# Kernel tuning notes

Hardware: AMD Instinct MI355X
Metric: run time of the kernel (lower is better)

The kernel has to match this reference:

```python
import jax, jax.numpy as jnp
import numpy as np

B = 131072

def _lin(x, w, b):
    return x @ w.T + b

def setup_inputs() -> dict:
    key = jax.random.key(0)
    ks = jax.random.split(key, 32)
    def rn(k, shape, scale=0.05):
        return jax.random.normal(k, shape, dtype=jnp.float32) * scale
    inp = {
        "x": rn(ks[0], (B, 256), 1.0),
        "w": rn(ks[1], (B, 36), 1.0),
        "h0": rn(ks[2], (B, 32), 1.0),
        "c0": rn(ks[3], (B, 32), 1.0),
        "fc1_w": rn(ks[4], (128, 256)), "fc1_b": rn(ks[5], (128,)),
        "fc1a_w": rn(ks[6], (128, 164)), "fc1a_b": rn(ks[7], (128,)),
        "fc1b_w": rn(ks[8], (128, 128)), "fc1b_b": rn(ks[9], (128,)),
        "w_game": rn(ks[10], (1, 12), 1.0),
        "fc1c_w": rn(ks[11], (64, 140)), "fc1c_b": rn(ks[12], (64,)),
        "fc2_w": rn(ks[13], (32, 64)), "fc2_b": rn(ks[14], (32,)),
        "fc3_w": rn(ks[15], (32, 32)), "fc3_b": rn(ks[16], (32,)),
        "w_ih": rn(ks[17], (128, 32)), "w_hh": rn(ks[18], (128, 32)),
        "b_ih": rn(ks[19], (128,)), "b_hh": rn(ks[20], (128,)),
        "fc4_w": rn(ks[21], (32, 32)), "fc4_b": rn(ks[22], (32,)),
        "fc5_w": rn(ks[23], (1, 32)), "fc5_b": rn(ks[24], (1,)),
    }
    return inp

def reference(x, w, h0, c0, fc1_w, fc1_b, fc1a_w, fc1a_b, fc1b_w, fc1b_b,
              w_game, fc1c_w, fc1c_b, fc2_w, fc2_b, fc3_w, fc3_b,
              w_ih, w_hh, b_ih, b_hh, fc4_w, fc4_b, fc5_w, fc5_b):
    b = x.shape[0]
    h = jax.nn.relu(_lin(x, fc1_w, fc1_b))                      # [B,128]
    h = jnp.concatenate([h, w], axis=-1)                        # [B,164]
    h = jax.nn.relu(_lin(h, fc1a_w, fc1a_b))                    # [B,128]
    h = jax.nn.relu(_lin(h, fc1b_w, fc1b_b))                    # [B,128]
    wg = jnp.broadcast_to(w_game.reshape(1, 12), (b, 12))
    h = jnp.concatenate([h, wg], axis=-1)                       # [B,140]
    h = jax.nn.relu(_lin(h, fc1c_w, fc1c_b))                    # [B,64]
    h = jax.nn.relu(_lin(h, fc2_w, fc2_b))                      # [B,32]
    h = jax.nn.relu(_lin(h, fc3_w, fc3_b))                      # [B,32]
    # LSTMCell step (torch gate order: input, forget, cell, output)
    gates = _lin(h, w_ih, b_ih) + _lin(h0, w_hh, b_hh)          # [B,128]
    i_g, f_g, g_g, o_g = jnp.split(gates, 4, axis=-1)
    c_new = jax.nn.sigmoid(f_g) * c0 + jax.nn.sigmoid(i_g) * jnp.tanh(g_g)
    h_new = jax.nn.sigmoid(o_g) * jnp.tanh(c_new)               # [B,32]
    out = jax.nn.relu(_lin(h_new, fc4_w, fc4_b))                # [B,32]
    out = _lin(out, fc5_w, fc5_b)                               # [B,1]
    return jax.nn.sigmoid(out)
```

## Files before the change

### kernel.cpp

```cpp
#include <hip/hip_runtime.h>
#include <hip/hip_bf16.h>


typedef __bf16 bf16x8 __attribute__((ext_vector_type(8)));
typedef float  f32x4  __attribute__((ext_vector_type(4)));
typedef int    i32x4  __attribute__((ext_vector_type(4)));

#define MFMA16(A, B, C) __builtin_amdgcn_mfma_f32_16x16x32_bf16((A), (B), (C), 0, 0, 0)

#define WOFF_FC1    0
#define WOFF_FC1A_H 32768
#define WOFF_FC1B   49152
#define WOFF_FC1C   65536
#define LDS_ELEMS   73728
#define WOFF_FC1A_W 73728
#define WOFF_FC2    81920
#define WOFF_FC3    83968
#define WOFF_WIH    84992
#define WOFF_WHH    89088
#define WOFF_FC4    93184
#define WTOT        94208
#define BOFF_FC1  0
#define BOFF_FC1A 128
#define BOFF_FC1B 256
#define BOFF_FC1C 384
#define BOFF_FC2  448
#define BOFF_FC3  480
#define BOFF_LSTM 512
#define BOFF_FC4  640
#define BTOT      672

__device__ __forceinline__ void conv_frag(int rel, const float* __restrict__ src,
                                          __bf16* __restrict__ dst,
                                          int ns, int Krow, int kbase, int klim, int perm) {
    int j    = rel & 7;
    int lane = (rel >> 3) & 63;
    int fs   = rel >> 9;
    int s    = fs % ns;
    int t    = fs / ns;
    int gq   = lane >> 4;
    int n    = 16 * t + (lane & 15);
    int k    = perm ? (16 * (2 * s + (j >> 2)) + 4 * gq + (j & 3))
                    : (32 * s + 8 * gq + j);
    float v  = (k < klim) ? src[n * Krow + kbase + k] : 0.f;
    dst[rel] = (__bf16)v;
}

__global__ void prep_kernel(const float* __restrict__ fc1w,  const float* __restrict__ fc1b,
                            const float* __restrict__ fc1aw, const float* __restrict__ fc1ab,
                            const float* __restrict__ fc1bw, const float* __restrict__ fc1bb,
                            const float* __restrict__ wgame, const float* __restrict__ fc1cw,
                            const float* __restrict__ fc1cb, const float* __restrict__ fc2w,
                            const float* __restrict__ fc2b,  const float* __restrict__ fc3w,
                            const float* __restrict__ fc3b,  const float* __restrict__ wih,
                            const float* __restrict__ whh,   const float* __restrict__ bih,
                            const float* __restrict__ bhh,   const float* __restrict__ fc4w,
                            const float* __restrict__ fc4b,
                            __bf16* __restrict__ wsw, float* __restrict__ wsb) {
    int idx = blockIdx.x * 256 + threadIdx.x;
    if (idx < WTOT) {
        if      (idx < WOFF_FC1A_H) conv_frag(idx - WOFF_FC1,    fc1w,  wsw + WOFF_FC1,    8, 256,   0, 256, 0);
        else if (idx < WOFF_FC1B)   conv_frag(idx - WOFF_FC1A_H, fc1aw, wsw + WOFF_FC1A_H, 4, 164,   0, 128, 1);
        else if (idx < WOFF_FC1C)   conv_frag(idx - WOFF_FC1B,   fc1bw, wsw + WOFF_FC1B,   4, 128,   0, 128, 1);
        else if (idx < WOFF_FC1A_W) conv_frag(idx - WOFF_FC1C,   fc1cw, wsw + WOFF_FC1C,   4, 140,   0, 128, 1);
        else if (idx < WOFF_FC2)    conv_frag(idx - WOFF_FC1A_W, fc1aw, wsw + WOFF_FC1A_W, 2, 164, 128,  36, 0);
        else if (idx < WOFF_FC3)    conv_frag(idx - WOFF_FC2,    fc2w,  wsw + WOFF_FC2,    2,  64,   0,  64, 1);
        else if (idx < WOFF_WIH)    conv_frag(idx - WOFF_FC3,    fc3w,  wsw + WOFF_FC3,    1,  32,   0,  32, 1);
        else if (idx < WOFF_WHH)    conv_frag(idx - WOFF_WIH,    wih,   wsw + WOFF_WIH,    1,  32,   0,  32, 1);
        else if (idx < WOFF_FC4)    conv_frag(idx - WOFF_WHH,    whh,   wsw + WOFF_WHH,    1,  32,   0,  32, 0);
        else                        conv_frag(idx - WOFF_FC4,    fc4w,  wsw + WOFF_FC4,    1,  32,   0,  32, 1);
    } else if (idx < WTOT + BTOT) {
        int bi = idx - WTOT;
        float v;
        if      (bi < 128) v = fc1b[bi];
        else if (bi < 256) v = fc1ab[bi - 128];
        else if (bi < 384) v = fc1bb[bi - 256];
        else if (bi < 448) {
            int n = bi - 384;
            v = fc1cb[n];
            for (int q = 0; q < 12; ++q) v += fc1cw[n * 140 + 128 + q] * wgame[q];
        }
        else if (bi < 480) v = fc2b[bi - 448];
        else if (bi < 512) v = fc3b[bi - 480];
        else if (bi < 640) { int n = bi - 512; v = bih[n] + bhh[n]; }
        else               v = fc4b[bi - 640];
        wsb[bi] = v;
    }
}

__device__ __forceinline__ bf16x8 ld8f(const float* __restrict__ p) {
    f32x4 a = *(const f32x4*)p;
    f32x4 b = *(const f32x4*)(p + 4);
    bf16x8 r;
    r[0] = (__bf16)a[0]; r[1] = (__bf16)a[1]; r[2] = (__bf16)a[2]; r[3] = (__bf16)a[3];
    r[4] = (__bf16)b[0]; r[5] = (__bf16)b[1]; r[6] = (__bf16)b[2]; r[7] = (__bf16)b[3];
    return r;
}

__device__ __forceinline__ bf16x8 ld4f_masked(const float* __restrict__ p, bool on) {
    f32x4 v = {0.f, 0.f, 0.f, 0.f};
    if (on) v = *(const f32x4*)p;
    bf16x8 r;
    r[0] = (__bf16)v[0]; r[1] = (__bf16)v[1]; r[2] = (__bf16)v[2]; r[3] = (__bf16)v[3];
    r[4] = (__bf16)0.f;  r[5] = (__bf16)0.f;  r[6] = (__bf16)0.f;  r[7] = (__bf16)0.f;
    return r;
}

__device__ __forceinline__ bf16x8 packrelu(const f32x4* a, int s) {
    bf16x8 r;
#pragma unroll
    for (int j = 0; j < 8; ++j) {
        float v = a[2 * s + (j >> 2)][j & 3];
        r[j] = (__bf16)fmaxf(v, 0.f);
    }
    return r;
}

__device__ __forceinline__ float sigm(float v)  { return 1.f / (1.f + __expf(-v)); }
__device__ __forceinline__ float tanh_(float v) { return 1.f - 2.f / (1.f + __expf(2.f * v)); }

__global__ __launch_bounds__(1024, 4) void fused_mlp_lstm(
        const float* __restrict__ x,  const float* __restrict__ w,
        const float* __restrict__ h0, const float* __restrict__ c0,
        const float* __restrict__ fc5w, const float* __restrict__ fc5b,
        const __bf16* __restrict__ wsw, const float* __restrict__ wsb,
        float* __restrict__ out) {
    __shared__ __align__(16) __bf16 slds[LDS_ELEMS];

    const int tid     = threadIdx.x;
    const int lane    = tid & 63;
    const int gq      = lane >> 4;
    const int mr      = lane & 15;
    const int rowbase = blockIdx.x * 256 + (tid >> 6) * 16;
    const int row     = rowbase + mr;

    {
        const i32x4* gs = (const i32x4*)wsw;
        i32x4*       sd = (i32x4*)slds;
#pragma unroll
        for (int i = 0; i < 9; ++i) sd[i * 1024 + tid] = gs[i * 1024 + tid];
    }
    __syncthreads();

    const bf16x8* Wfc1  = (const bf16x8*)(slds + WOFF_FC1);
    const bf16x8* Wf1aH = (const bf16x8*)(slds + WOFF_FC1A_H);
    const bf16x8* Wfc1b = (const bf16x8*)(slds + WOFF_FC1B);
    const bf16x8* Wfc1c = (const bf16x8*)(slds + WOFF_FC1C);
    const bf16x8* Wf1aW = (const bf16x8*)(wsw + WOFF_FC1A_W);
    const bf16x8* Wfc2  = (const bf16x8*)(wsw + WOFF_FC2);
    const bf16x8* Wfc3  = (const bf16x8*)(wsw + WOFF_FC3);
    const bf16x8* Wwih  = (const bf16x8*)(wsw + WOFF_WIH);
    const bf16x8* Wwhh  = (const bf16x8*)(wsw + WOFF_WHH);
    const bf16x8* Wfc4  = (const bf16x8*)(wsw + WOFF_FC4);

    bf16x8 h1f[4];
    {
        f32x4 acc1[8];
#pragma unroll
        for (int t = 0; t < 8; ++t)
            acc1[t] = *(const f32x4*)(wsb + BOFF_FC1 + 16 * t + 4 * gq);
        const float* xrow = x + row * 256 + 8 * gq;
#pragma unroll
        for (int p = 0; p < 4; ++p) {
            bf16x8 a0 = ld8f(xrow + 64 * p);
            bf16x8 a1 = ld8f(xrow + 64 * p + 32);
#pragma unroll
            for (int t = 0; t < 8; ++t)
                acc1[t] = MFMA16(Wfc1[(t * 8 + 2 * p) * 64 + lane], a0, acc1[t]);
#pragma unroll
            for (int t = 0; t < 8; ++t)
                acc1[t] = MFMA16(Wfc1[(t * 8 + 2 * p + 1) * 64 + lane], a1, acc1[t]);
        }
#pragma unroll
        for (int s = 0; s < 4; ++s) h1f[s] = packrelu(acc1, s);
    }

    bf16x8 h2f[4];
    {
        bf16x8 wxa0 = ld8f(w + row * 36 + 8 * gq);
        bf16x8 wxa1 = ld4f_masked(w + row * 36 + 32, gq == 0);
        f32x4 acc2[8];
#pragma unroll
        for (int t = 0; t < 8; ++t)
            acc2[t] = *(const f32x4*)(wsb + BOFF_FC1A + 16 * t + 4 * gq);
#pragma unroll
        for (int s = 0; s < 4; ++s)
#pragma unroll
            for (int t = 0; t < 8; ++t)
                acc2[t] = MFMA16(Wf1aH[(t * 4 + s) * 64 + lane], h1f[s], acc2[t]);
#pragma unroll
        for (int t = 0; t < 8; ++t) {
            acc2[t] = MFMA16(Wf1aW[(t * 2 + 0) * 64 + lane], wxa0, acc2[t]);
            acc2[t] = MFMA16(Wf1aW[(t * 2 + 1) * 64 + lane], wxa1, acc2[t]);
        }
#pragma unroll
        for (int s = 0; s < 4; ++s) h2f[s] = packrelu(acc2, s);
    }

    bf16x8 h3f[4];
    {
        f32x4 acc3[8];
#pragma unroll
        for (int t = 0; t < 8; ++t)
            acc3[t] = *(const f32x4*)(wsb + BOFF_FC1B + 16 * t + 4 * gq);
#pragma unroll
        for (int s = 0; s < 4; ++s)
#pragma unroll
            for (int t = 0; t < 8; ++t)
                acc3[t] = MFMA16(Wfc1b[(t * 4 + s) * 64 + lane], h2f[s], acc3[t]);
#pragma unroll
        for (int s = 0; s < 4; ++s) h3f[s] = packrelu(acc3, s);
    }

    bf16x8 h0f  = ld8f(h0 + row * 32 + 8 * gq);
    f32x4  c0r0 = *(const f32x4*)(c0 + row * 32 + 4 * gq);
    f32x4  c0r1 = *(const f32x4*)(c0 + row * 32 + 16 + 4 * gq);

    bf16x8 h4f[2];
    {
        f32x4 acc4[4];
#pragma unroll
        for (int t = 0; t < 4; ++t)
            acc4[t] = *(const f32x4*)(wsb + BOFF_FC1C + 16 * t + 4 * gq);
#pragma unroll
        for (int s = 0; s < 4; ++s)
#pragma unroll
            for (int t = 0; t < 4; ++t)
                acc4[t] = MFMA16(Wfc1c[(t * 4 + s) * 64 + lane], h3f[s], acc4[t]);
#pragma unroll
        for (int s = 0; s < 2; ++s) h4f[s] = packrelu(acc4, s);
    }

    bf16x8 h5f;
    {
        f32x4 acc5[2];
#pragma unroll
        for (int t = 0; t < 2; ++t)
            acc5[t] = *(const f32x4*)(wsb + BOFF_FC2 + 16 * t + 4 * gq);
#pragma unroll
        for (int s = 0; s < 2; ++s)
#pragma unroll
            for (int t = 0; t < 2; ++t)
                acc5[t] = MFMA16(Wfc2[(t * 2 + s) * 64 + lane], h4f[s], acc5[t]);
        h5f = packrelu(acc5, 0);
    }

    bf16x8 h6f;
    {
        f32x4 acc6[2];
#pragma unroll
        for (int t = 0; t < 2; ++t)
            acc6[t] = *(const f32x4*)(wsb + BOFF_FC3 + 16 * t + 4 * gq);
#pragma unroll
        for (int t = 0; t < 2; ++t)
            acc6[t] = MFMA16(Wfc3[t * 64 + lane], h5f, acc6[t]);
        h6f = packrelu(acc6, 0);
    }

    bf16x8 hnf;
    {
        f32x4 accg[8];
#pragma unroll
        for (int t = 0; t < 8; ++t)
            accg[t] = *(const f32x4*)(wsb + BOFF_LSTM + 16 * t + 4 * gq);
#pragma unroll
        for (int t = 0; t < 8; ++t)
            accg[t] = MFMA16(Wwih[t * 64 + lane], h6f, accg[t]);
#pragma unroll
        for (int t = 0; t < 8; ++t)
            accg[t] = MFMA16(Wwhh[t * 64 + lane], h0f, accg[t]);
#pragma unroll
        for (int t2 = 0; t2 < 2; ++t2) {
            f32x4 cc = t2 ? c0r1 : c0r0;
#pragma unroll
            for (int r = 0; r < 4; ++r) {
                float ig = accg[t2][r];
                float fg = accg[2 + t2][r];
                float gg = accg[4 + t2][r];
                float og = accg[6 + t2][r];
                float cn = sigm(fg) * cc[r] + sigm(ig) * tanh_(gg);
                hnf[t2 * 4 + r] = (__bf16)(sigm(og) * tanh_(cn));
            }
        }
    }

    f32x4 acco[2];
#pragma unroll
    for (int t = 0; t < 2; ++t)
        acco[t] = *(const f32x4*)(wsb + BOFF_FC4 + 16 * t + 4 * gq);
#pragma unroll
    for (int t = 0; t < 2; ++t)
        acco[t] = MFMA16(Wfc4[t * 64 + lane], hnf, acco[t]);

    f32x4 w5a = *(const f32x4*)(fc5w + 4 * gq);
    f32x4 w5b = *(const f32x4*)(fc5w + 16 + 4 * gq);
    float p = 0.f;
#pragma unroll
    for (int r = 0; r < 4; ++r) {
        p += fmaxf(acco[0][r], 0.f) * w5a[r];
        p += fmaxf(acco[1][r], 0.f) * w5b[r];
    }
    p += __shfl_xor(p, 16);
    p += __shfl_xor(p, 32);
    float res = sigm(p + fc5b[0]);
    if (lane < 16) out[rowbase + lane] = res;
}

extern "C" void kernel_launch(void* const* d_in, const int* in_sizes, int n_in,
                              void* d_out, int out_size, void* d_ws, size_t ws_size,
                              hipStream_t stream) {
    const float* x     = (const float*)d_in[0];
    const float* w     = (const float*)d_in[1];
    const float* h0    = (const float*)d_in[2];
    const float* c0    = (const float*)d_in[3];
    const float* fc1w  = (const float*)d_in[4];
    const float* fc1b  = (const float*)d_in[5];
    const float* fc1aw = (const float*)d_in[6];
    const float* fc1ab = (const float*)d_in[7];
    const float* fc1bw = (const float*)d_in[8];
    const float* fc1bb = (const float*)d_in[9];
    const float* wgame = (const float*)d_in[10];
    const float* fc1cw = (const float*)d_in[11];
    const float* fc1cb = (const float*)d_in[12];
    const float* fc2w  = (const float*)d_in[13];
    const float* fc2b  = (const float*)d_in[14];
    const float* fc3w  = (const float*)d_in[15];
    const float* fc3b  = (const float*)d_in[16];
    const float* wih   = (const float*)d_in[17];
    const float* whh   = (const float*)d_in[18];
    const float* bih   = (const float*)d_in[19];
    const float* bhh   = (const float*)d_in[20];
    const float* fc4w  = (const float*)d_in[21];
    const float* fc4b  = (const float*)d_in[22];
    const float* fc5w  = (const float*)d_in[23];
    const float* fc5b  = (const float*)d_in[24];

    __bf16* wsw = (__bf16*)d_ws;
    float*  wsb = (float*)((char*)d_ws + WTOT * sizeof(__bf16));
    (void)ws_size; (void)n_in; (void)out_size;

    const int Btot = in_sizes[0] / 256;

    prep_kernel<<<(WTOT + BTOT + 255) / 256, 256, 0, stream>>>(
        fc1w, fc1b, fc1aw, fc1ab, fc1bw, fc1bb, wgame, fc1cw, fc1cb,
        fc2w, fc2b, fc3w, fc3b, wih, whh, bih, bhh, fc4w, fc4b, wsw, wsb);

    fused_mlp_lstm<<<Btot / 256, 1024, 0, stream>>>(
        x, w, h0, c0, fc5w, fc5b, wsw, wsb, (float*)d_out);
}
```

Baseline: 61.42 us.

## Split fused MLP-LSTM into three kernels with LDS-resident weights

Splits the single fused kernel into three stage kernels (fc1, fc1a+fc1b, tail through LSTM and output). Each stage keeps only its own weights in LDS, and each wave processes two 16-row tiles so every weight fragment read from LDS feeds two MFMAs. The aim is to cut LDS footprint per block, which raises occupancy, and to keep the tail weights out of global memory. The cost is a bf16 round-trip of the h1 and h3 activations through workspace (tens of MB of extra traffic) plus extra launches. The old fused kernel is kept as a fallback when the workspace is too small.

```diff
diff --git a/kernel.cpp b/kernel.cpp
--- a/kernel.cpp
+++ b/kernel.cpp
@@ -12,7 +12,6 @@
 #define WOFF_FC1A_H 32768
 #define WOFF_FC1B   49152
 #define WOFF_FC1C   65536
-#define LDS_ELEMS   73728
 #define WOFF_FC1A_W 73728
 #define WOFF_FC2    81920
 #define WOFF_FC3    83968
@@ -29,6 +28,10 @@
 #define BOFF_LSTM 512
 #define BOFF_FC4  640
 #define BTOT      672
+
+#define H1_BYTE_OFF 192512ull
+#define HACT_BYTES  33554432ull
+#define WS_REQUIRED (H1_BYTE_OFF + 2ull * HACT_BYTES)
 
 __device__ __forceinline__ void conv_frag(int rel, const float* __restrict__ src,
                                           __bf16* __restrict__ dst,
@@ -119,6 +122,310 @@
 __device__ __forceinline__ float sigm(float v)  { return 1.f / (1.f + __expf(-v)); }
 __device__ __forceinline__ float tanh_(float v) { return 1.f - 2.f / (1.f + __expf(2.f * v)); }
 
+__global__ __launch_bounds__(512, 2) void k_l1(
+        const float* __restrict__ x, const __bf16* __restrict__ wsw,
+        const float* __restrict__ wsb, __bf16* __restrict__ h1ws) {
+    __shared__ __align__(16) __bf16 slds[32768];
+    const int tid  = threadIdx.x;
+    const int lane = tid & 63;
+    const int wv   = tid >> 6;
+    const int gq   = lane >> 4;
+    const int mr   = lane & 15;
+    {
+        const i32x4* gs = (const i32x4*)(wsw + WOFF_FC1);
+        i32x4*       sd = (i32x4*)slds;
+#pragma unroll
+        for (int i = 0; i < 8; ++i) sd[i * 512 + tid] = gs[i * 512 + tid];
+    }
+    __syncthreads();
+    const bf16x8* Wfc1 = (const bf16x8*)slds;
+
+    const int rowbase = blockIdx.x * 256 + wv * 32;
+    const int rowA = rowbase + mr, rowB = rowA + 16;
+    f32x4 aA[8], aB[8];
+#pragma unroll
+    for (int t = 0; t < 8; ++t) {
+        f32x4 bv = *(const f32x4*)(wsb + BOFF_FC1 + 16 * t + 4 * gq);
+        aA[t] = bv; aB[t] = bv;
+    }
+    const float* xrA = x + rowA * 256 + 8 * gq;
+    const float* xrB = x + rowB * 256 + 8 * gq;
+#pragma unroll
+    for (int p = 0; p < 4; ++p) {
+        bf16x8 a0A = ld8f(xrA + 64 * p);
+        bf16x8 a0B = ld8f(xrB + 64 * p);
+        bf16x8 a1A = ld8f(xrA + 64 * p + 32);
+        bf16x8 a1B = ld8f(xrB + 64 * p + 32);
+#pragma unroll
+        for (int t = 0; t < 8; ++t) {
+            bf16x8 wf = Wfc1[(t * 8 + 2 * p) * 64 + lane];
+            aA[t] = MFMA16(wf, a0A, aA[t]);
+            aB[t] = MFMA16(wf, a0B, aB[t]);
+        }
+#pragma unroll
+        for (int t = 0; t < 8; ++t) {
+            bf16x8 wf = Wfc1[(t * 8 + 2 * p + 1) * 64 + lane];
+            aA[t] = MFMA16(wf, a1A, aA[t]);
+            aB[t] = MFMA16(wf, a1B, aB[t]);
+        }
+    }
+    const int rb = rowbase >> 4;
+#pragma unroll
+    for (int s = 0; s < 4; ++s) {
+        *(bf16x8*)(h1ws + ((rb * 4 + s) * 512)       + lane * 8) = packrelu(aA, s);
+        *(bf16x8*)(h1ws + (((rb + 1) * 4 + s) * 512) + lane * 8) = packrelu(aB, s);
+    }
+}
+
+__global__ __launch_bounds__(512, 2) void k_l1ab(
+        const float* __restrict__ w, const __bf16* __restrict__ wsw,
+        const float* __restrict__ wsb, const __bf16* __restrict__ h1ws,
+        __bf16* __restrict__ h3ws) {
+    __shared__ __align__(16) __bf16 slds[40960];
+    const int tid  = threadIdx.x;
+    const int lane = tid & 63;
+    const int wv   = tid >> 6;
+    const int gq   = lane >> 4;
+    const int mr   = lane & 15;
+    const int rowbase = blockIdx.x * 256 + wv * 32;
+    const int rowA = rowbase + mr, rowB = rowA + 16;
+    const int rb = rowbase >> 4;
+
+    bf16x8 h1fA[4], h1fB[4];
+#pragma unroll
+    for (int s = 0; s < 4; ++s) {
+        h1fA[s] = *(const bf16x8*)(h1ws + ((rb * 4 + s) * 512)       + lane * 8);
+        h1fB[s] = *(const bf16x8*)(h1ws + (((rb + 1) * 4 + s) * 512) + lane * 8);
+    }
+    bf16x8 wxa0 = ld8f(w + rowA * 36 + 8 * gq);
+    bf16x8 wxb0 = ld8f(w + rowB * 36 + 8 * gq);
+    bf16x8 wxa1 = ld4f_masked(w + rowA * 36 + 32, gq == 0);
+    bf16x8 wxb1 = ld4f_masked(w + rowB * 36 + 32, gq == 0);
+
+    {
+        const i32x4* g1 = (const i32x4*)(wsw + WOFF_FC1A_H);
+        const i32x4* g2 = (const i32x4*)(wsw + WOFF_FC1A_W);
+        i32x4*       sd = (i32x4*)slds;
+#pragma unroll
+        for (int i = 0; i < 8; ++i) sd[i * 512 + tid] = g1[i * 512 + tid];
+#pragma unroll
+        for (int i = 0; i < 2; ++i) sd[4096 + i * 512 + tid] = g2[i * 512 + tid];
+    }
+    __syncthreads();
+    const bf16x8* Wf1aH = (const bf16x8*)(slds);
+    const bf16x8* Wfc1b = (const bf16x8*)(slds + 16384);
+    const bf16x8* Wf1aW = (const bf16x8*)(slds + 32768);
+
+    f32x4 aA[8], aB[8];
+#pragma unroll
+    for (int t = 0; t < 8; ++t) {
+        f32x4 bv = *(const f32x4*)(wsb + BOFF_FC1A + 16 * t + 4 * gq);
+        aA[t] = bv; aB[t] = bv;
+    }
+#pragma unroll
+    for (int s = 0; s < 4; ++s)
+#pragma unroll
+        for (int t = 0; t < 8; ++t) {
+            bf16x8 wf = Wf1aH[(t * 4 + s) * 64 + lane];
+            aA[t] = MFMA16(wf, h1fA[s], aA[t]);
+            aB[t] = MFMA16(wf, h1fB[s], aB[t]);
+        }
+#pragma unroll
+    for (int t = 0; t < 8; ++t) {
+        bf16x8 wf0 = Wf1aW[(t * 2 + 0) * 64 + lane];
+        bf16x8 wf1 = Wf1aW[(t * 2 + 1) * 64 + lane];
+        aA[t] = MFMA16(wf0, wxa0, aA[t]);
+        aB[t] = MFMA16(wf0, wxb0, aB[t]);
+        aA[t] = MFMA16(wf1, wxa1, aA[t]);
+        aB[t] = MFMA16(wf1, wxb1, aB[t]);
+    }
+    bf16x8 h2fA[4], h2fB[4];
+#pragma unroll
+    for (int s = 0; s < 4; ++s) { h2fA[s] = packrelu(aA, s); h2fB[s] = packrelu(aB, s); }
+
+    f32x4 bA[8], bB[8];
+#pragma unroll
+    for (int t = 0; t < 8; ++t) {
+        f32x4 bv = *(const f32x4*)(wsb + BOFF_FC1B + 16 * t + 4 * gq);
+        bA[t] = bv; bB[t] = bv;
+    }
+#pragma unroll
+    for (int s = 0; s < 4; ++s)
+#pragma unroll
+        for (int t = 0; t < 8; ++t) {
+            bf16x8 wf = Wfc1b[(t * 4 + s) * 64 + lane];
+            bA[t] = MFMA16(wf, h2fA[s], bA[t]);
+            bB[t] = MFMA16(wf, h2fB[s], bB[t]);
+        }
+#pragma unroll
+    for (int s = 0; s < 4; ++s) {
+        *(bf16x8*)(h3ws + ((rb * 4 + s) * 512)       + lane * 8) = packrelu(bA, s);
+        *(bf16x8*)(h3ws + (((rb + 1) * 4 + s) * 512) + lane * 8) = packrelu(bB, s);
+    }
+}
+
+__global__ __launch_bounds__(512, 2) void k_tail(
+        const float* __restrict__ h0, const float* __restrict__ c0,
+        const float* __restrict__ fc5w, const float* __restrict__ fc5b,
+        const __bf16* __restrict__ wsw, const float* __restrict__ wsb,
+        const __bf16* __restrict__ h3ws, float* __restrict__ out) {
+    __shared__ __align__(16) __bf16 slds[28672];
+    const int tid  = threadIdx.x;
+    const int lane = tid & 63;
+    const int wv   = tid >> 6;
+    const int gq   = lane >> 4;
+    const int mr   = lane & 15;
+    const int rowbase = blockIdx.x * 256 + wv * 32;
+    const int rowA = rowbase + mr, rowB = rowA + 16;
+    const int rb = rowbase >> 4;
+
+    bf16x8 h3fA[4], h3fB[4];
+#pragma unroll
+    for (int s = 0; s < 4; ++s) {
+        h3fA[s] = *(const bf16x8*)(h3ws + ((rb * 4 + s) * 512)       + lane * 8);
+        h3fB[s] = *(const bf16x8*)(h3ws + (((rb + 1) * 4 + s) * 512) + lane * 8);
+    }
+    bf16x8 h0fA = ld8f(h0 + rowA * 32 + 8 * gq);
+    bf16x8 h0fB = ld8f(h0 + rowB * 32 + 8 * gq);
+    f32x4  cA0 = *(const f32x4*)(c0 + rowA * 32 + 4 * gq);
+    f32x4  cA1 = *(const f32x4*)(c0 + rowA * 32 + 16 + 4 * gq);
+    f32x4  cB0 = *(const f32x4*)(c0 + rowB * 32 + 4 * gq);
+    f32x4  cB1 = *(const f32x4*)(c0 + rowB * 32 + 16 + 4 * gq);
+
+    {
+        const i32x4* gs = (const i32x4*)(wsw + WOFF_FC1C);
+        i32x4*       sd = (i32x4*)slds;
+#pragma unroll
+        for (int i = 0; i < 7; ++i) sd[i * 512 + tid] = gs[i * 512 + tid];
+    }
+    __syncthreads();
+    const bf16x8* Wfc1c = (const bf16x8*)(slds);
+    const bf16x8* Wfc2  = (const bf16x8*)(slds + 16384);
+    const bf16x8* Wfc3  = (const bf16x8*)(slds + 18432);
+    const bf16x8* Wwih  = (const bf16x8*)(slds + 19456);
+    const bf16x8* Wwhh  = (const bf16x8*)(slds + 23552);
+    const bf16x8* Wfc4  = (const bf16x8*)(slds + 27648);
+
+    bf16x8 h4fA[2], h4fB[2];
+    {
+        f32x4 aA[4], aB[4];
+#pragma unroll
+        for (int t = 0; t < 4; ++t) {
+            f32x4 bv = *(const f32x4*)(wsb + BOFF_FC1C + 16 * t + 4 * gq);
+            aA[t] = bv; aB[t] = bv;
+        }
+#pragma unroll
+        for (int s = 0; s < 4; ++s)
+#pragma unroll
+            for (int t = 0; t < 4; ++t) {
+                bf16x8 wf = Wfc1c[(t * 4 + s) * 64 + lane];
+                aA[t] = MFMA16(wf, h3fA[s], aA[t]);
+                aB[t] = MFMA16(wf, h3fB[s], aB[t]);
+            }
+#pragma unroll
+        for (int s = 0; s < 2; ++s) { h4fA[s] = packrelu(aA, s); h4fB[s] = packrelu(aB, s); }
+    }
+    bf16x8 h5fA, h5fB;
+    {
+        f32x4 aA[2], aB[2];
+#pragma unroll
+        for (int t = 0; t < 2; ++t) {
+            f32x4 bv = *(const f32x4*)(wsb + BOFF_FC2 + 16 * t + 4 * gq);
+            aA[t] = bv; aB[t] = bv;
+        }
+#pragma unroll
+        for (int s = 0; s < 2; ++s)
+#pragma unroll
+            for (int t = 0; t < 2; ++t) {
+                bf16x8 wf = Wfc2[(t * 2 + s) * 64 + lane];
+                aA[t] = MFMA16(wf, h4fA[s], aA[t]);
+                aB[t] = MFMA16(wf, h4fB[s], aB[t]);
+            }
+        h5fA = packrelu(aA, 0); h5fB = packrelu(aB, 0);
+    }
+    bf16x8 h6fA, h6fB;
+    {
+        f32x4 aA[2], aB[2];
+#pragma unroll
+        for (int t = 0; t < 2; ++t) {
+            f32x4 bv = *(const f32x4*)(wsb + BOFF_FC3 + 16 * t + 4 * gq);
+            aA[t] = bv; aB[t] = bv;
+        }
+#pragma unroll
+        for (int t = 0; t < 2; ++t) {
+            bf16x8 wf = Wfc3[t * 64 + lane];
+            aA[t] = MFMA16(wf, h5fA, aA[t]);
+            aB[t] = MFMA16(wf, h5fB, aB[t]);
+        }
+        h6fA = packrelu(aA, 0); h6fB = packrelu(aB, 0);
+    }
+    bf16x8 hnfA, hnfB;
+    {
+        f32x4 gA[8], gB[8];
+#pragma unroll
+        for (int t = 0; t < 8; ++t) {
+            f32x4 bv = *(const f32x4*)(wsb + BOFF_LSTM + 16 * t + 4 * gq);
+            gA[t] = bv; gB[t] = bv;
+        }
+#pragma unroll
+        for (int t = 0; t < 8; ++t) {
+            bf16x8 wf = Wwih[t * 64 + lane];
+            gA[t] = MFMA16(wf, h6fA, gA[t]);
+            gB[t] = MFMA16(wf, h6fB, gB[t]);
+        }
+#pragma unroll
+        for (int t = 0; t < 8; ++t) {
+            bf16x8 wf = Wwhh[t * 64 + lane];
+            gA[t] = MFMA16(wf, h0fA, gA[t]);
+            gB[t] = MFMA16(wf, h0fB, gB[t]);
+        }
+#pragma unroll
+        for (int t2 = 0; t2 < 2; ++t2) {
+            f32x4 ccA = t2 ? cA1 : cA0;
+            f32x4 ccB = t2 ? cB1 : cB0;
+#pragma unroll
+            for (int r = 0; r < 4; ++r) {
+                float cnA = sigm(gA[2 + t2][r]) * ccA[r] + sigm(gA[t2][r]) * tanh_(gA[4 + t2][r]);
+                float cnB = sigm(gB[2 + t2][r]) * ccB[r] + sigm(gB[t2][r]) * tanh_(gB[4 + t2][r]);
+                hnfA[t2 * 4 + r] = (__bf16)(sigm(gA[6 + t2][r]) * tanh_(cnA));
+                hnfB[t2 * 4 + r] = (__bf16)(sigm(gB[6 + t2][r]) * tanh_(cnB));
+            }
+        }
+    }
+    f32x4 oA[2], oB[2];
+#pragma unroll
+    for (int t = 0; t < 2; ++t) {
+        f32x4 bv = *(const f32x4*)(wsb + BOFF_FC4 + 16 * t + 4 * gq);
+        oA[t] = bv; oB[t] = bv;
+    }
+#pragma unroll
+    for (int t = 0; t < 2; ++t) {
+        bf16x8 wf = Wfc4[t * 64 + lane];
+        oA[t] = MFMA16(wf, hnfA, oA[t]);
+        oB[t] = MFMA16(wf, hnfB, oB[t]);
+    }
+    f32x4 w5a = *(const f32x4*)(fc5w + 4 * gq);
+    f32x4 w5b = *(const f32x4*)(fc5w + 16 + 4 * gq);
+    float b5  = fc5b[0];
+    float pA = 0.f, pB = 0.f;
+#pragma unroll
+    for (int r = 0; r < 4; ++r) {
+        pA += fmaxf(oA[0][r], 0.f) * w5a[r];
+        pA += fmaxf(oA[1][r], 0.f) * w5b[r];
+        pB += fmaxf(oB[0][r], 0.f) * w5a[r];
+        pB += fmaxf(oB[1][r], 0.f) * w5b[r];
+    }
+    pA += __shfl_xor(pA, 16); pA += __shfl_xor(pA, 32);
+    pB += __shfl_xor(pB, 16); pB += __shfl_xor(pB, 32);
+    float resA = sigm(pA + b5);
+    float resB = sigm(pB + b5);
+    if (lane < 16) {
+        out[rowbase + lane]      = resA;
+        out[rowbase + 16 + lane] = resB;
+    }
+}
+
+#define LDS_ELEMS 73728
 __global__ __launch_bounds__(1024, 4) void fused_mlp_lstm(
         const float* __restrict__ x,  const float* __restrict__ w,
         const float* __restrict__ h0, const float* __restrict__ c0,
@@ -126,14 +433,12 @@
         const __bf16* __restrict__ wsw, const float* __restrict__ wsb,
         float* __restrict__ out) {
     __shared__ __align__(16) __bf16 slds[LDS_ELEMS];
-
     const int tid     = threadIdx.x;
     const int lane    = tid & 63;
     const int gq      = lane >> 4;
     const int mr      = lane & 15;
     const int rowbase = blockIdx.x * 256 + (tid >> 6) * 16;
     const int row     = rowbase + mr;
-
     {
         const i32x4* gs = (const i32x4*)wsw;
         i32x4*       sd = (i32x4*)slds;
@@ -141,7 +446,6 @@
         for (int i = 0; i < 9; ++i) sd[i * 1024 + tid] = gs[i * 1024 + tid];
     }
     __syncthreads();
-
     const bf16x8* Wfc1  = (const bf16x8*)(slds + WOFF_FC1);
     const bf16x8* Wf1aH = (const bf16x8*)(slds + WOFF_FC1A_H);
     const bf16x8* Wfc1b = (const bf16x8*)(slds + WOFF_FC1B);
@@ -152,7 +456,6 @@
     const bf16x8* Wwih  = (const bf16x8*)(wsw + WOFF_WIH);
     const bf16x8* Wwhh  = (const bf16x8*)(wsw + WOFF_WHH);
     const bf16x8* Wfc4  = (const bf16x8*)(wsw + WOFF_FC4);
-
     bf16x8 h1f[4];
     {
         f32x4 acc1[8];
@@ -174,7 +477,6 @@
 #pragma unroll
         for (int s = 0; s < 4; ++s) h1f[s] = packrelu(acc1, s);
     }
-
     bf16x8 h2f[4];
     {
         bf16x8 wxa0 = ld8f(w + row * 36 + 8 * gq);
@@ -196,7 +498,6 @@
 #pragma unroll
         for (int s = 0; s < 4; ++s) h2f[s] = packrelu(acc2, s);
     }
-
     bf16x8 h3f[4];
     {
         f32x4 acc3[8];
@@ -211,11 +512,9 @@
 #pragma unroll
         for (int s = 0; s < 4; ++s) h3f[s] = packrelu(acc3, s);
     }
-
     bf16x8 h0f  = ld8f(h0 + row * 32 + 8 * gq);
     f32x4  c0r0 = *(const f32x4*)(c0 + row * 32 + 4 * gq);
     f32x4  c0r1 = *(const f32x4*)(c0 + row * 32 + 16 + 4 * gq);
-
     bf16x8 h4f[2];
     {
         f32x4 acc4[4];
@@ -230,7 +529,6 @@
 #pragma unroll
         for (int s = 0; s < 2; ++s) h4f[s] = packrelu(acc4, s);
     }
-
     bf16x8 h5f;
     {
         f32x4 acc5[2];
@@ -244,7 +542,6 @@
                 acc5[t] = MFMA16(Wfc2[(t * 2 + s) * 64 + lane], h4f[s], acc5[t]);
         h5f = packrelu(acc5, 0);
     }
-
     bf16x8 h6f;
     {
         f32x4 acc6[2];
@@ -256,7 +553,6 @@
             acc6[t] = MFMA16(Wfc3[t * 64 + lane], h5f, acc6[t]);
         h6f = packrelu(acc6, 0);
     }
-
     bf16x8 hnf;
     {
         f32x4 accg[8];
@@ -283,7 +579,6 @@
             }
         }
     }
-
     f32x4 acco[2];
 #pragma unroll
     for (int t = 0; t < 2; ++t)
@@ -291,7 +586,6 @@
 #pragma unroll
     for (int t = 0; t < 2; ++t)
         acco[t] = MFMA16(Wfc4[t * 64 + lane], hnf, acco[t]);
-
     f32x4 w5a = *(const f32x4*)(fc5w + 4 * gq);
     f32x4 w5b = *(const f32x4*)(fc5w + 16 + 4 * gq);
     float p = 0.f;
@@ -337,7 +631,7 @@
 
     __bf16* wsw = (__bf16*)d_ws;
     float*  wsb = (float*)((char*)d_ws + WTOT * sizeof(__bf16));
-    (void)ws_size; (void)n_in; (void)out_size;
+    (void)n_in; (void)out_size;
 
     const int Btot = in_sizes[0] / 256;
 
@@ -345,6 +639,14 @@
         fc1w, fc1b, fc1aw, fc1ab, fc1bw, fc1bb, wgame, fc1cw, fc1cb,
         fc2w, fc2b, fc3w, fc3b, wih, whh, bih, bhh, fc4w, fc4b, wsw, wsb);
 
-    fused_mlp_lstm<<<Btot / 256, 1024, 0, stream>>>(
-        x, w, h0, c0, fc5w, fc5b, wsw, wsb, (float*)d_out);
-}
+    if (ws_size >= WS_REQUIRED) {
+        __bf16* h1ws = (__bf16*)((char*)d_ws + H1_BYTE_OFF);
+        __bf16* h3ws = (__bf16*)((char*)d_ws + H1_BYTE_OFF + HACT_BYTES);
+        k_l1  <<<Btot / 256, 512, 0, stream>>>(x, wsw, wsb, h1ws);
+        k_l1ab<<<Btot / 256, 512, 0, stream>>>(w, wsw, wsb, h1ws, h3ws);
+        k_tail<<<Btot / 256, 512, 0, stream>>>(h0, c0, fc5w, fc5b, wsw, wsb, h3ws, (float*)d_out);
+    } else {
+        fused_mlp_lstm<<<Btot / 256, 1024, 0, stream>>>(
+            x, w, h0, c0, fc5w, fc5b, wsw, wsb, (float*)d_out);
+    }
+}
```

New measurement: 87.70 us. 42.8% more time.
